# Kernel tuning notes

Hardware: AMD Instinct MI355X
Metric: run time of the kernel (lower is better)

## Reference

```python
import jax, jax.numpy as jnp
import numpy as np
import math

N = 100000
D = 128      # input_dim
H = 4        # heads
DK = 32      # d_k
DV = D // H  # d_v = 32


def setup_inputs() -> dict:
    key = jax.random.key(0)
    k1, k2, k3, k4, k5 = jax.random.split(key, 5)
    x = jax.random.normal(k1, (N, D), dtype=jnp.float32)
    neighbor_index = jax.random.randint(k2, (N, 4), 0, N, dtype=jnp.int64)
    w_q = jax.random.normal(k3, (H, D, DK), dtype=jnp.float32) * 0.05
    w_k = jax.random.normal(k4, (H, 5, D, DK), dtype=jnp.float32) * 0.05
    w_v = jax.random.normal(k5, (H, 5, D, DV), dtype=jnp.float32) * 0.05
    return {"x": x, "neighbor_index": neighbor_index, "w_q": w_q, "w_k": w_k, "w_v": w_v}


def reference(x, neighbor_index, w_q, w_k, w_v):
    n = x.shape[0]
    d_k = w_q.shape[-1]
    # gather 4 neighbors, prepend self node -> (N, 5, D)
    x_neighbors = jnp.concatenate([x[:, None, :], x[neighbor_index]], axis=1)
    Q = jnp.einsum('nd,hdk->hnk', x, w_q)                 # (H, N, DK)
    K = jnp.einsum('nrd,hrdk->hnrk', x_neighbors, w_k)    # (H, N, 5, DK)
    V = jnp.einsum('nrd,hrdv->hnrv', x_neighbors, w_v)    # (H, N, 5, DV)
    A = jnp.einsum('hnk,hnrk->hnr', Q, K) / math.sqrt(d_k)
    # NOTE: original torch code applies softmax over dim=1, which is the NODE
    # dimension (not the neighbor dimension r). Replicated faithfully.
    A = jax.nn.softmax(A, axis=1)
    Z = jnp.einsum('hnr,hnrv->hnv', A, V)                 # (H, N, DV)
    return Z.transpose(1, 0, 2).reshape(n, -1)            # (N, H*DV)
```

## Files before the change

kernel.cpp:

```cpp
#include <hip/hip_runtime.h>


#define N_NODES 100000
#define D 128
#define H 4
#define R 5
#define NPB 32
#define THREADS 256
#define NBLOCKS (N_NODES / NPB)

typedef _Float16 half_t;
typedef __attribute__((ext_vector_type(2))) _Float16 f16x2;
typedef __attribute__((ext_vector_type(8))) _Float16 f16x8;
typedef __attribute__((ext_vector_type(4))) float f32x4;

typedef const __attribute__((address_space(1))) unsigned int* gp_t;
typedef __attribute__((address_space(3))) unsigned int* lp_t;

__device__ __forceinline__ void async_copy16(const void* g, void* l) {
    __builtin_amdgcn_global_load_lds((gp_t)g, (lp_t)l, 16, 0, 0);
}

__global__ void prep(const float* __restrict__ x,
                     const float* __restrict__ wq, const float* __restrict__ wk,
                     const float* __restrict__ wv,
                     half_t* __restrict__ xh, half_t* __restrict__ wph,
                     float* __restrict__ sums_p)
{
    const int bid = blockIdx.x;
    const int t = threadIdx.x;
    if (bid < 44) {
        const float* src = (bid < 4) ? (wq + bid * 4096)
                         : (bid < 24) ? (wk + (bid - 4) * 4096)
                                      : (wv + (bid - 24) * 4096);
#pragma unroll
        for (int i = 0; i < 16; ++i) {
            int p = t * 16 + i;
            int j = p & 7, ln = (p >> 3) & 63, f = p >> 9;
            int kt = f & 3, mt = f >> 2;
            int d = kt * 32 + (ln >> 4) * 8 + j;
            int ko = mt * 16 + (ln & 15);
            wph[bid * 4096 + p] = (half_t)src[d * 32 + ko];
        }
    } else {
        if (bid == 44) {
            for (int i = t; i < 1280; i += THREADS) sums_p[i] = 0.f;
        }
        const int total = N_NODES * D / 8;
        const int nb = gridDim.x - 44;
        for (int i = (bid - 44) * THREADS + t; i < total; i += nb * THREADS) {
            const float4* s = (const float4*)x + (size_t)i * 2;
            float4 a = s[0], b = s[1];
            f16x8 h8 = {(half_t)a.x, (half_t)a.y, (half_t)a.z, (half_t)a.w,
                        (half_t)b.x, (half_t)b.y, (half_t)b.z, (half_t)b.w};
            *((f16x8*)xh + i) = h8;
        }
    }
}

__device__ __forceinline__ void stage_all(const half_t* __restrict__ xh,
                                          const int* __restrict__ nbr,
                                          int base, char* tile, int tid)
{
    const int w = tid >> 6;
    const int lane = tid & 63;
    const int rr = lane >> 4, c = lane & 15;
    const int rowA = w * 4 + rr;
    const int rowB = rowA + 16;
    const int nodeA = base + rowA;
    const int nodeB = base + rowB;
    int4 a4 = ((const int4*)nbr)[nodeA];
    int4 b4 = ((const int4*)nbr)[nodeB];
    int srcA[5] = {nodeA, a4.x, a4.y, a4.z, a4.w};
    int srcB[5] = {nodeB, b4.x, b4.y, b4.z, b4.w};
    const int sw = ((c ^ (rowA & 7)) << 4);
#pragma unroll
    for (int s = 0; s < 5; ++s) {
        const char* gA = (const char*)xh + (size_t)srcA[s] * 256 + sw;
        const char* gB = (const char*)xh + (size_t)srcB[s] * 256 + sw;
        async_copy16(gA, tile + s * 8192 + (w * 4) * 256);
        async_copy16(gB, tile + s * 8192 + (w * 4 + 16) * 256);
    }
}

__device__ __forceinline__ void load_af(int mid, const half_t* __restrict__ wph,
                                        int lane, f16x8 (&af)[8])
{
#pragma unroll
    for (int kt = 0; kt < 4; ++kt) {
        af[kt * 2]     = *(const f16x8*)(wph + ((mid * 8 + kt) * 64 + lane) * 8);
        af[kt * 2 + 1] = *(const f16x8*)(wph + ((mid * 8 + 4 + kt) * 64 + lane) * 8);
    }
}

__device__ __forceinline__ void proj32(const f16x8 (&af)[8], const half_t* tile,
                                       int lane, f32x4 (&acc)[2][2])
{
    const int l15 = lane & 15, q = lane >> 4;
#pragma unroll
    for (int mt = 0; mt < 2; ++mt)
#pragma unroll
        for (int nt = 0; nt < 2; ++nt)
            acc[mt][nt] = (f32x4){0.f, 0.f, 0.f, 0.f};
#pragma unroll
    for (int kt = 0; kt < 4; ++kt) {
#pragma unroll
        for (int nt = 0; nt < 2; ++nt) {
            int row = nt * 16 + l15;
            int sq = (kt * 4 + q) ^ (row & 7);
            f16x8 b = *(const f16x8*)(tile + row * 128 + sq * 8);
            acc[0][nt] = __builtin_amdgcn_mfma_f32_16x16x32_f16(af[kt * 2], b, acc[0][nt], 0, 0, 0);
            acc[1][nt] = __builtin_amdgcn_mfma_f32_16x16x32_f16(af[kt * 2 + 1], b, acc[1][nt], 0, 0, 0);
        }
    }
}

__global__ __launch_bounds__(THREADS, 4)
void knot_logits(const half_t* __restrict__ xh, const int* __restrict__ nbr,
                 const half_t* __restrict__ wph,
                 half_t* __restrict__ eh, float* __restrict__ sums_p)
{
    __shared__ __align__(16) char smem[5 * 8192];
    const int base = blockIdx.x * NPB;
    const int lane = threadIdx.x & 63;
    const int h = __builtin_amdgcn_readfirstlane((int)(threadIdx.x >> 6));
    const int l15 = lane & 15, q = lane >> 4;

    stage_all(xh, nbr, base, smem, threadIdx.x);

    f16x8 af[8];
    load_af(h, wph, lane, af);
    __syncthreads();

    f32x4 qf[2][2], kf[2][2];
    proj32(af, (const half_t*)smem, lane, qf);

    f16x2 epk[5];
    float esum[5];
#pragma unroll
    for (int r = 0; r < R; ++r) {
        load_af(4 + h * 5 + r, wph, lane, af);
        proj32(af, (const half_t*)(smem + r * 8192), lane, kf);

        float es = 0.f;
#pragma unroll
        for (int nt = 0; nt < 2; ++nt) {
            float p = 0.f;
#pragma unroll
            for (int mt = 0; mt < 2; ++mt)
#pragma unroll
                for (int j = 0; j < 4; ++j)
                    p += qf[mt][nt][j] * kf[mt][nt][j];
            p += __shfl_xor(p, 16, 64);
            p += __shfl_xor(p, 32, 64);
            float e = __expf(p * 0.17677669529663688f);
            epk[r][nt] = (half_t)e;
            es += e;
        }
        es += __shfl_xor(es, 1, 64); es += __shfl_xor(es, 2, 64);
        es += __shfl_xor(es, 4, 64); es += __shfl_xor(es, 8, 64);
        esum[r] = es;
    }

#pragma unroll
    for (int r = 0; r < R; ++r) {
        if (q == 0) {
#pragma unroll
            for (int nt = 0; nt < 2; ++nt)
                eh[(size_t)(h * 5 + r) * N_NODES + base + nt * 16 + l15] = epk[r][nt];
        }
        if (lane == 0)
            atomicAdd(&sums_p[(h * 5 + r) * 64 + (blockIdx.x & 63)], esum[r]);
    }
}

#define ZS 132
__global__ __launch_bounds__(THREADS, 4)
void knot_out(const half_t* __restrict__ xh, const int* __restrict__ nbr,
              const half_t* __restrict__ wph, const half_t* __restrict__ eh,
              const float* __restrict__ sums_p, float* __restrict__ out)
{
    __shared__ __align__(16) char smem[5 * 8192];
    const int base = blockIdx.x * NPB;
    const int lane = threadIdx.x & 63;
    const int h = __builtin_amdgcn_readfirstlane((int)(threadIdx.x >> 6));
    const int l15 = lane & 15, q = lane >> 4;

    stage_all(xh, nbr, base, smem, threadIdx.x);

    float inv[5];
#pragma unroll
    for (int r = 0; r < R; ++r) {
        float v = sums_p[(h * 5 + r) * 64 + lane];
        v += __shfl_xor(v, 1, 64);  v += __shfl_xor(v, 2, 64);
        v += __shfl_xor(v, 4, 64);  v += __shfl_xor(v, 8, 64);
        v += __shfl_xor(v, 16, 64); v += __shfl_xor(v, 32, 64);
        inv[r] = 1.0f / v;
    }
    float ev[5][2];
#pragma unroll
    for (int r = 0; r < R; ++r)
#pragma unroll
        for (int nt = 0; nt < 2; ++nt)
            ev[r][nt] = (float)eh[(size_t)(h * 5 + r) * N_NODES + base + nt * 16 + l15];

    f16x8 af[8];
    load_af(24 + h * 5 + 0, wph, lane, af);
    __syncthreads();

    f32x4 z[2][2], vf[2][2];
#pragma unroll
    for (int mt = 0; mt < 2; ++mt)
#pragma unroll
        for (int nt = 0; nt < 2; ++nt)
            z[mt][nt] = (f32x4){0.f, 0.f, 0.f, 0.f};

#pragma unroll
    for (int r = 0; r < R; ++r) {
        proj32(af, (const half_t*)(smem + r * 8192), lane, vf);
        if (r < R - 1) load_af(24 + h * 5 + r + 1, wph, lane, af);
#pragma unroll
        for (int nt = 0; nt < 2; ++nt) {
            float w = ev[r][nt] * inv[r];
#pragma unroll
            for (int mt = 0; mt < 2; ++mt)
#pragma unroll
                for (int j = 0; j < 4; ++j)
                    z[mt][nt][j] += w * vf[mt][nt][j];
        }
    }

    __syncthreads();
    float* zt = (float*)smem;
#pragma unroll
    for (int mt = 0; mt < 2; ++mt)
#pragma unroll
        for (int nt = 0; nt < 2; ++nt) {
            int node = nt * 16 + l15;
            int col = h * 32 + mt * 16 + q * 4;
            *(f32x4*)(zt + node * ZS + col) = z[mt][nt];
        }
    __syncthreads();
    {
        const int row = threadIdx.x >> 3;
        const int c = threadIdx.x & 7;
        float* dst = out + (size_t)(base + row) * D + c * 16;
        const float* srcp = zt + row * ZS + c * 16;
#pragma unroll
        for (int i4 = 0; i4 < 4; ++i4)
            *(float4*)(dst + i4 * 4) = *(const float4*)(srcp + i4 * 4);
    }
}

extern "C" void kernel_launch(void* const* d_in, const int* in_sizes, int n_in,
                              void* d_out, int out_size, void* d_ws, size_t ws_size,
                              hipStream_t stream)
{
    const float* x   = (const float*)d_in[0];
    const int*   nbr = (const int*)d_in[1];
    const float* w_q = (const float*)d_in[2];
    const float* w_k = (const float*)d_in[3];
    const float* w_v = (const float*)d_in[4];
    float* out = (float*)d_out;

    float*  sums_p = (float*)d_ws;
    half_t* eh     = (half_t*)((char*)d_ws + 8192);
    half_t* wph    = (half_t*)((char*)d_ws + 4194304);
    half_t* xh     = (half_t*)((char*)d_ws + 4718592);

    prep<<<44 + 2048, THREADS, 0, stream>>>(x, w_q, w_k, w_v, xh, wph, sums_p);
    knot_logits<<<NBLOCKS, THREADS, 0, stream>>>(xh, nbr, wph, eh, sums_p);
    knot_out<<<NBLOCKS, THREADS, 0, stream>>>(xh, nbr, wph, eh, sums_p, out);
}
```

Measured before the change: 184.4 us.

## Make logits and output kernels persistent with double-buffered async gather staging

Both attention kernels now launch a fixed grid of persistent blocks that walk over 32-node tiles. The next tile's neighbour indices are prefetched and its gathered rows are staged into a second LDS buffer while the current tile is projected, so gather latency overlaps MFMA work. Projection weights for several neighbour slots stay resident in registers across tiles, and per-block softmax sums accumulate before a single atomic. The output kernel writes results straight from registers instead of transposing through LDS. The cost is more registers and LDS per block, which lowers occupancy (launch bounds go from 4 to 2 blocks), and the scattered direct stores may coalesce less well.

```diff
diff --git a/kernel.cpp b/kernel.cpp
--- a/kernel.cpp
+++ b/kernel.cpp
@@ -6,11 +6,13 @@
 #define H 4
 #define R 5
 #define NPB 32
+#define NT 3125
+#define GRID 1024
 #define THREADS 256
-#define NBLOCKS (N_NODES / NPB)
+#define TILE_B 8192
+#define BUF_B (5 * TILE_B)
 
 typedef _Float16 half_t;
-typedef __attribute__((ext_vector_type(2))) _Float16 f16x2;
 typedef __attribute__((ext_vector_type(8))) _Float16 f16x8;
 typedef __attribute__((ext_vector_type(4))) float f32x4;
 
@@ -19,6 +21,34 @@
 
 __device__ __forceinline__ void async_copy16(const void* g, void* l) {
     __builtin_amdgcn_global_load_lds((gp_t)g, (lp_t)l, 16, 0, 0);
+}
+
+struct NB { int4 a, b; };
+
+__device__ __forceinline__ NB ld_nb(const int* __restrict__ nbr, int base, int tid) {
+    int rowA = ((tid >> 6) << 2) + ((tid & 63) >> 4);
+    NB nb;
+    nb.a = ((const int4*)nbr)[base + rowA];
+    nb.b = ((const int4*)nbr)[base + rowA + 16];
+    return nb;
+}
+
+__device__ __forceinline__ void stage_all(const half_t* __restrict__ xh, int base,
+                                          const NB& nb, char* tile, int tid)
+{
+    const int w = tid >> 6, lane = tid & 63;
+    const int rr = lane >> 4, c = lane & 15;
+    const int rowA = (w << 2) + rr;
+    int srcA[5] = {base + rowA, nb.a.x, nb.a.y, nb.a.z, nb.a.w};
+    int srcB[5] = {base + rowA + 16, nb.b.x, nb.b.y, nb.b.z, nb.b.w};
+    const int sw = ((c ^ (rowA & 7)) << 4);
+#pragma unroll
+    for (int s = 0; s < 5; ++s) {
+        async_copy16((const char*)xh + (size_t)srcA[s] * 256 + sw,
+                     tile + s * TILE_B + (w * 4) * 256);
+        async_copy16((const char*)xh + (size_t)srcB[s] * 256 + sw,
+                     tile + s * TILE_B + (w * 4 + 16) * 256);
+    }
 }
 
 __global__ void prep(const float* __restrict__ x,
@@ -58,31 +88,6 @@
     }
 }
 
-__device__ __forceinline__ void stage_all(const half_t* __restrict__ xh,
-                                          const int* __restrict__ nbr,
-                                          int base, char* tile, int tid)
-{
-    const int w = tid >> 6;
-    const int lane = tid & 63;
-    const int rr = lane >> 4, c = lane & 15;
-    const int rowA = w * 4 + rr;
-    const int rowB = rowA + 16;
-    const int nodeA = base + rowA;
-    const int nodeB = base + rowB;
-    int4 a4 = ((const int4*)nbr)[nodeA];
-    int4 b4 = ((const int4*)nbr)[nodeB];
-    int srcA[5] = {nodeA, a4.x, a4.y, a4.z, a4.w};
-    int srcB[5] = {nodeB, b4.x, b4.y, b4.z, b4.w};
-    const int sw = ((c ^ (rowA & 7)) << 4);
-#pragma unroll
-    for (int s = 0; s < 5; ++s) {
-        const char* gA = (const char*)xh + (size_t)srcA[s] * 256 + sw;
-        const char* gB = (const char*)xh + (size_t)srcB[s] * 256 + sw;
-        async_copy16(gA, tile + s * 8192 + (w * 4) * 256);
-        async_copy16(gB, tile + s * 8192 + (w * 4 + 16) * 256);
-    }
-}
-
 __device__ __forceinline__ void load_af(int mid, const half_t* __restrict__ wph,
                                         int lane, f16x8 (&af)[8])
 {
@@ -115,78 +120,138 @@
     }
 }
 
-__global__ __launch_bounds__(THREADS, 4)
+__device__ __forceinline__ void proj32_2(const f16x8 (&a0)[8], const f16x8 (&a1)[8],
+                                         const half_t* tile, int lane,
+                                         f32x4 (&c0)[2][2], f32x4 (&c1)[2][2])
+{
+    const int l15 = lane & 15, q = lane >> 4;
+#pragma unroll
+    for (int mt = 0; mt < 2; ++mt)
+#pragma unroll
+        for (int nt = 0; nt < 2; ++nt) {
+            c0[mt][nt] = (f32x4){0.f, 0.f, 0.f, 0.f};
+            c1[mt][nt] = (f32x4){0.f, 0.f, 0.f, 0.f};
+        }
+#pragma unroll
+    for (int kt = 0; kt < 4; ++kt) {
+#pragma unroll
+        for (int nt = 0; nt < 2; ++nt) {
+            int row = nt * 16 + l15;
+            int sq = (kt * 4 + q) ^ (row & 7);
+            f16x8 b = *(const f16x8*)(tile + row * 128 + sq * 8);
+            c0[0][nt] = __builtin_amdgcn_mfma_f32_16x16x32_f16(a0[kt * 2], b, c0[0][nt], 0, 0, 0);
+            c0[1][nt] = __builtin_amdgcn_mfma_f32_16x16x32_f16(a0[kt * 2 + 1], b, c0[1][nt], 0, 0, 0);
+            c1[0][nt] = __builtin_amdgcn_mfma_f32_16x16x32_f16(a1[kt * 2], b, c1[0][nt], 0, 0, 0);
+            c1[1][nt] = __builtin_amdgcn_mfma_f32_16x16x32_f16(a1[kt * 2 + 1], b, c1[1][nt], 0, 0, 0);
+        }
+    }
+}
+
+#define LOGIT(r)                                                              \
+    {   float es_ = 0.f;                                                      \
+        _Pragma("unroll")                                                     \
+        for (int nt = 0; nt < 2; ++nt) {                                      \
+            float p_ = 0.f;                                                   \
+            _Pragma("unroll")                                                 \
+            for (int mt = 0; mt < 2; ++mt)                                    \
+                _Pragma("unroll")                                             \
+                for (int j = 0; j < 4; ++j)                                   \
+                    p_ += qf[mt][nt][j] * kf[mt][nt][j];                      \
+            p_ += __shfl_xor(p_, 16, 64);                                     \
+            p_ += __shfl_xor(p_, 32, 64);                                     \
+            float e_ = __expf(p_ * 0.17677669529663688f);                     \
+            if (q == 0)                                                       \
+                eh[(size_t)(h * 5 + (r)) * N_NODES + base + nt * 16 + l15] = (half_t)e_; \
+            es_ += e_;                                                        \
+        }                                                                     \
+        es_ += __shfl_xor(es_, 1, 64); es_ += __shfl_xor(es_, 2, 64);         \
+        es_ += __shfl_xor(es_, 4, 64); es_ += __shfl_xor(es_, 8, 64);         \
+        esum_acc[r] += es_;                                                   \
+    }
+
+__global__ __launch_bounds__(THREADS, 2)
 void knot_logits(const half_t* __restrict__ xh, const int* __restrict__ nbr,
                  const half_t* __restrict__ wph,
                  half_t* __restrict__ eh, float* __restrict__ sums_p)
 {
-    __shared__ __align__(16) char smem[5 * 8192];
-    const int base = blockIdx.x * NPB;
-    const int lane = threadIdx.x & 63;
-    const int h = __builtin_amdgcn_readfirstlane((int)(threadIdx.x >> 6));
+    __shared__ __align__(16) char smem[2 * BUF_B];
+    const int tid = threadIdx.x;
+    const int lane = tid & 63;
+    const int h = __builtin_amdgcn_readfirstlane((int)(tid >> 6));
     const int l15 = lane & 15, q = lane >> 4;
 
-    stage_all(xh, nbr, base, smem, threadIdx.x);
-
-    f16x8 af[8];
-    load_af(h, wph, lane, af);
+    f16x8 aq[8], ak0[8], ak1[8], ak2[8];
+    load_af(h, wph, lane, aq);
+    load_af(4 + h * 5 + 0, wph, lane, ak0);
+    load_af(4 + h * 5 + 1, wph, lane, ak1);
+    load_af(4 + h * 5 + 2, wph, lane, ak2);
+
+    float esum_acc[5] = {0.f, 0.f, 0.f, 0.f, 0.f};
+
+    int t = blockIdx.x;
+    char* cur = smem;
+    char* nxt = smem + BUF_B;
+    {
+        NB nb0 = ld_nb(nbr, t * NPB, tid);
+        stage_all(xh, t * NPB, nb0, cur, tid);
+    }
+    int tn = t + GRID;
+    bool hasn = (tn < NT);
+    NB nb_n;
+    if (hasn) nb_n = ld_nb(nbr, tn * NPB, tid);
     __syncthreads();
 
-    f32x4 qf[2][2], kf[2][2];
-    proj32(af, (const half_t*)smem, lane, qf);
-
-    f16x2 epk[5];
-    float esum[5];
-#pragma unroll
-    for (int r = 0; r < R; ++r) {
-        load_af(4 + h * 5 + r, wph, lane, af);
-        proj32(af, (const half_t*)(smem + r * 8192), lane, kf);
-
-        float es = 0.f;
-#pragma unroll
-        for (int nt = 0; nt < 2; ++nt) {
-            float p = 0.f;
-#pragma unroll
-            for (int mt = 0; mt < 2; ++mt)
-#pragma unroll
-                for (int j = 0; j < 4; ++j)
-                    p += qf[mt][nt][j] * kf[mt][nt][j];
-            p += __shfl_xor(p, 16, 64);
-            p += __shfl_xor(p, 32, 64);
-            float e = __expf(p * 0.17677669529663688f);
-            epk[r][nt] = (half_t)e;
-            es += e;
-        }
-        es += __shfl_xor(es, 1, 64); es += __shfl_xor(es, 2, 64);
-        es += __shfl_xor(es, 4, 64); es += __shfl_xor(es, 8, 64);
-        esum[r] = es;
-    }
-
-#pragma unroll
-    for (int r = 0; r < R; ++r) {
-        if (q == 0) {
-#pragma unroll
-            for (int nt = 0; nt < 2; ++nt)
-                eh[(size_t)(h * 5 + r) * N_NODES + base + nt * 16 + l15] = epk[r][nt];
-        }
+#pragma unroll 1
+    for (;;) {
+        const int base = t * NPB;
+        if (hasn) stage_all(xh, tn * NPB, nb_n, nxt, tid);
+        const int tn2 = tn + GRID;
+        if (tn2 < NT) nb_n = ld_nb(nbr, tn2 * NPB, tid);
+
+        f16x8 pb[8];
+        load_af(4 + h * 5 + 3, wph, lane, pb);
+
+        f32x4 qf[2][2], kf[2][2];
+        const half_t* tp = (const half_t*)cur;
+        proj32_2(aq, ak0, tp, lane, qf, kf);
+        LOGIT(0)
+        proj32(ak1, (const half_t*)(cur + TILE_B), lane, kf);     LOGIT(1)
+        proj32(ak2, (const half_t*)(cur + 2 * TILE_B), lane, kf); LOGIT(2)
+        proj32(pb,  (const half_t*)(cur + 3 * TILE_B), lane, kf); LOGIT(3)
+        load_af(4 + h * 5 + 4, wph, lane, pb);
+        proj32(pb,  (const half_t*)(cur + 4 * TILE_B), lane, kf); LOGIT(4)
+
+        if (!hasn) break;
+        __syncthreads();
+        { char* tmp = cur; cur = nxt; nxt = tmp; }
+        t = tn; tn = tn2; hasn = (tn < NT);
+    }
+
+#pragma unroll
+    for (int r = 0; r < R; ++r)
         if (lane == 0)
-            atomicAdd(&sums_p[(h * 5 + r) * 64 + (blockIdx.x & 63)], esum[r]);
-    }
-}
-
-#define ZS 132
-__global__ __launch_bounds__(THREADS, 4)
+            atomicAdd(&sums_p[(h * 5 + r) * 64 + (blockIdx.x & 63)], esum_acc[r]);
+}
+
+#define VACC(r)                                                               \
+    _Pragma("unroll")                                                         \
+    for (int nt = 0; nt < 2; ++nt) {                                          \
+        float w_ = evc[r][nt] * inv[r];                                       \
+        _Pragma("unroll")                                                     \
+        for (int mt = 0; mt < 2; ++mt)                                        \
+            z[mt][nt] += w_ * vf[mt][nt];                                     \
+    }
+
+__global__ __launch_bounds__(THREADS, 2)
 void knot_out(const half_t* __restrict__ xh, const int* __restrict__ nbr,
               const half_t* __restrict__ wph, const half_t* __restrict__ eh,
               const float* __restrict__ sums_p, float* __restrict__ out)
 {
-    __shared__ __align__(16) char smem[5 * 8192];
-    const int base = blockIdx.x * NPB;
-    const int lane = threadIdx.x & 63;
-    const int h = __builtin_amdgcn_readfirstlane((int)(threadIdx.x >> 6));
+    __shared__ __align__(16) char smem[2 * BUF_B];
+    const int tid = threadIdx.x;
+    const int lane = tid & 63;
+    const int h = __builtin_amdgcn_readfirstlane((int)(tid >> 6));
     const int l15 = lane & 15, q = lane >> 4;
-
-    stage_all(xh, nbr, base, smem, threadIdx.x);
 
     float inv[5];
 #pragma unroll
@@ -197,58 +262,84 @@
         v += __shfl_xor(v, 16, 64); v += __shfl_xor(v, 32, 64);
         inv[r] = 1.0f / v;
     }
-    float ev[5][2];
+
+    f16x8 av0[8], av1[8], av2[8];
+    load_af(24 + h * 5 + 0, wph, lane, av0);
+    load_af(24 + h * 5 + 1, wph, lane, av1);
+    load_af(24 + h * 5 + 2, wph, lane, av2);
+
+    int t = blockIdx.x;
+    char* cur = smem;
+    char* nxt = smem + BUF_B;
+    {
+        NB nb0 = ld_nb(nbr, t * NPB, tid);
+        stage_all(xh, t * NPB, nb0, cur, tid);
+    }
+    int tn = t + GRID;
+    bool hasn = (tn < NT);
+    NB nb_n;
+    if (hasn) nb_n = ld_nb(nbr, tn * NPB, tid);
+    float evc[5][2];
 #pragma unroll
     for (int r = 0; r < R; ++r)
 #pragma unroll
         for (int nt = 0; nt < 2; ++nt)
-            ev[r][nt] = (float)eh[(size_t)(h * 5 + r) * N_NODES + base + nt * 16 + l15];
-
-    f16x8 af[8];
-    load_af(24 + h * 5 + 0, wph, lane, af);
+            evc[r][nt] = (float)eh[(size_t)(h * 5 + r) * N_NODES + t * NPB + nt * 16 + l15];
     __syncthreads();
 
-    f32x4 z[2][2], vf[2][2];
-#pragma unroll
-    for (int mt = 0; mt < 2; ++mt)
-#pragma unroll
-        for (int nt = 0; nt < 2; ++nt)
-            z[mt][nt] = (f32x4){0.f, 0.f, 0.f, 0.f};
-
-#pragma unroll
-    for (int r = 0; r < R; ++r) {
-        proj32(af, (const half_t*)(smem + r * 8192), lane, vf);
-        if (r < R - 1) load_af(24 + h * 5 + r + 1, wph, lane, af);
+#pragma unroll 1
+    for (;;) {
+        const int base = t * NPB;
+        if (hasn) stage_all(xh, tn * NPB, nb_n, nxt, tid);
+        const int tn2 = tn + GRID;
+        if (tn2 < NT) nb_n = ld_nb(nbr, tn2 * NPB, tid);
+
+        float evn[5][2];
+        if (hasn) {
+#pragma unroll
+            for (int r = 0; r < R; ++r)
+#pragma unroll
+                for (int nt = 0; nt < 2; ++nt)
+                    evn[r][nt] = (float)eh[(size_t)(h * 5 + r) * N_NODES + tn * NPB + nt * 16 + l15];
+        }
+
+        f16x8 pb[8];
+        load_af(24 + h * 5 + 3, wph, lane, pb);
+
+        f32x4 z[2][2], vf[2][2];
+        proj32(av0, (const half_t*)cur, lane, vf);
 #pragma unroll
         for (int nt = 0; nt < 2; ++nt) {
-            float w = ev[r][nt] * inv[r];
+            float w_ = evc[0][nt] * inv[0];
 #pragma unroll
             for (int mt = 0; mt < 2; ++mt)
-#pragma unroll
-                for (int j = 0; j < 4; ++j)
-                    z[mt][nt][j] += w * vf[mt][nt][j];
-        }
-    }
-
-    __syncthreads();
-    float* zt = (float*)smem;
-#pragma unroll
-    for (int mt = 0; mt < 2; ++mt)
-#pragma unroll
-        for (int nt = 0; nt < 2; ++nt) {
-            int node = nt * 16 + l15;
-            int col = h * 32 + mt * 16 + q * 4;
-            *(f32x4*)(zt + node * ZS + col) = z[mt][nt];
-        }
-    __syncthreads();
-    {
-        const int row = threadIdx.x >> 3;
-        const int c = threadIdx.x & 7;
-        float* dst = out + (size_t)(base + row) * D + c * 16;
-        const float* srcp = zt + row * ZS + c * 16;
-#pragma unroll
-        for (int i4 = 0; i4 < 4; ++i4)
-            *(float4*)(dst + i4 * 4) = *(const float4*)(srcp + i4 * 4);
+                z[mt][nt] = w_ * vf[mt][nt];
+        }
+        proj32(av1, (const half_t*)(cur + TILE_B), lane, vf);     VACC(1)
+        proj32(av2, (const half_t*)(cur + 2 * TILE_B), lane, vf); VACC(2)
+        proj32(pb,  (const half_t*)(cur + 3 * TILE_B), lane, vf); VACC(3)
+        load_af(24 + h * 5 + 4, wph, lane, pb);
+        proj32(pb,  (const half_t*)(cur + 4 * TILE_B), lane, vf); VACC(4)
+
+#pragma unroll
+        for (int mt = 0; mt < 2; ++mt)
+#pragma unroll
+            for (int nt = 0; nt < 2; ++nt) {
+                float* dst = out + (size_t)(base + nt * 16 + l15) * D
+                           + h * 32 + mt * 16 + q * 4;
+                *(float4*)dst = (float4){z[mt][nt][0], z[mt][nt][1],
+                                         z[mt][nt][2], z[mt][nt][3]};
+            }
+
+        if (!hasn) break;
+#pragma unroll
+        for (int r = 0; r < R; ++r) {
+            evc[r][0] = evn[r][0];
+            evc[r][1] = evn[r][1];
+        }
+        __syncthreads();
+        { char* tmp = cur; cur = nxt; nxt = tmp; }
+        t = tn; tn = tn2; hasn = (tn < NT);
     }
 }
 
@@ -269,6 +360,6 @@
     half_t* xh     = (half_t*)((char*)d_ws + 4718592);
 
     prep<<<44 + 2048, THREADS, 0, stream>>>(x, w_q, w_k, w_v, xh, wph, sums_p);
-    knot_logits<<<NBLOCKS, THREADS, 0, stream>>>(xh, nbr, wph, eh, sums_p);
-    knot_out<<<NBLOCKS, THREADS, 0, stream>>>(xh, nbr, wph, eh, sums_p, out);
-}
+    knot_logits<<<GRID, THREADS, 0, stream>>>(xh, nbr, wph, eh, sums_p);
+    knot_out<<<GRID, THREADS, 0, stream>>>(xh, nbr, wph, eh, sums_p, out);
+}
```

Result: slower. 194.1 us (+5.3%).
